# Performance work log

Hardware: AMD Instinct MI355X
Metric: run time of the kernel (lower is better)

## Reference

```python
import jax, jax.numpy as jnp
import numpy as np

B, S, D, H = 2, 2048, 1024, 16
HD = D // H  # head dim = 64


def setup_inputs() -> dict:
    key = jax.random.key(0)
    ks = jax.random.split(key, 8)
    s = 0.02
    return {
        "Q": jax.random.normal(ks[0], (B, S, D), jnp.float32),
        "K": jax.random.normal(ks[1], (B, S, D), jnp.float32),
        "V": jax.random.normal(ks[2], (B, S, D), jnp.float32),
        "mask": jax.random.randint(ks[3], (1, 1, S, S), 0, 2, jnp.int32),
        "Wq": jax.random.normal(ks[4], (D, D), jnp.float32) * s,
        "bq": jnp.zeros((D,), jnp.float32),
        "Wk": jax.random.normal(ks[5], (D, D), jnp.float32) * s,
        "bk": jnp.zeros((D,), jnp.float32),
        "Wv": jax.random.normal(ks[6], (D, D), jnp.float32) * s,
        "bv": jnp.zeros((D,), jnp.float32),
        "Wo": jax.random.normal(ks[7], (D, D), jnp.float32) * s,
        "bo": jnp.zeros((D,), jnp.float32),
    }


def reference(Q, K, V, mask, Wq, bq, Wk, bk, Wv, bv, Wo, bo):
    b = Q.shape[0]
    # QKV projections, split into heads: [B,S,D] -> [B,H,S,HD]
    q = (Q @ Wq + bq).reshape(b, -1, H, HD).transpose(0, 2, 1, 3)
    k = (K @ Wk + bk).reshape(b, -1, H, HD).transpose(0, 2, 1, 3)
    v = (V @ Wv + bv).reshape(b, -1, H, HD).transpose(0, 2, 1, 3)
    # scaled dot-product attention with full [B,H,S,S] scores (as in source)
    scale = jnp.sqrt(jnp.asarray(HD, q.dtype))
    scores = jnp.einsum("bhqd,bhkd->bhqk", q, k) / scale
    scores = jnp.where(mask == 0, -jnp.inf, scores)
    attn = jax.nn.softmax(scores, axis=-1)
    ctx = jnp.einsum("bhqk,bhkd->bhqd", attn, v)
    # merge heads and output projection
    concat = ctx.transpose(0, 2, 1, 3).reshape(b, -1, H * HD)
    return concat @ Wo + bo
```

## Files before the change

kernel.cpp:

```cpp
#include <hip/hip_runtime.h>


using s8v = __attribute__((ext_vector_type(8))) short;
using f4v = __attribute__((ext_vector_type(4))) float;
using f16v = __attribute__((ext_vector_type(16))) float;
typedef unsigned long long u64;

__device__ __forceinline__ unsigned short f2bf(float f) {
  union { float f; unsigned int u; } v; v.f = f;
  return (unsigned short)((v.u + 0x7fffu + ((v.u >> 16) & 1u)) >> 16);
}

__device__ __forceinline__ unsigned pkbf(float lo, float hi2) {
  return __builtin_amdgcn_perm(__float_as_uint(hi2), __float_as_uint(lo), 0x07060302);
}

__device__ __forceinline__ void gll16(const void* g, void* l) {
  __builtin_amdgcn_global_load_lds(
      (const __attribute__((address_space(1))) unsigned int*)g,
      (__attribute__((address_space(3))) unsigned int*)l, 16, 0, 0);
}

__global__ void prep_kernel(const float* __restrict__ Q, const float* __restrict__ K,
                            const float* __restrict__ V,
                            unsigned short* __restrict__ qb, unsigned short* __restrict__ kb,
                            unsigned short* __restrict__ vb,
                            const float* __restrict__ W0, const float* __restrict__ W1,
                            const float* __restrict__ W2, const float* __restrict__ W3,
                            unsigned short* __restrict__ T0, unsigned short* __restrict__ T1,
                            unsigned short* __restrict__ T2, unsigned short* __restrict__ T3,
                            const int* __restrict__ mask, unsigned* __restrict__ bmw) {
  __shared__ unsigned short t[64][72];
  const int bid = blockIdx.x, tid = threadIdx.x;
  if (bid < 1536) {
    int z = bid >> 9;
    int base = (bid & 511) * 2048;
    const float* in = (z == 0) ? Q : (z == 1) ? K : V;
    unsigned short* out = (z == 0) ? qb : (z == 1) ? kb : vb;
#pragma unroll
    for (int j = 0; j < 8; ++j) {
      int idx = base + j * 256 + tid;
      float4 v = ((const float4*)in)[idx];
      ushort4 o;
      o.x = f2bf(v.x); o.y = f2bf(v.y); o.z = f2bf(v.z); o.w = f2bf(v.w);
      ((ushort4*)out)[idx] = o;
    }
  } else if (bid < 2560) {
    int b = bid - 1536;
    int z = b >> 8, rem = b & 255;
    int k0 = (rem >> 4) * 64, n0 = (rem & 15) * 64;
    const float* W = (z == 0) ? W0 : (z == 1) ? W1 : (z == 2) ? W2 : W3;
    unsigned short* Wt = (z == 0) ? T0 : (z == 1) ? T1 : (z == 2) ? T2 : T3;
    for (int p = 0; p < 4; ++p) {
      int idx = p * 256 + tid;
      int row = idx >> 4, c4 = idx & 15;
      float4 v = *(const float4*)&W[(size_t)(k0 + row) * 1024 + n0 + c4 * 4];
      t[row][c4 * 4 + 0] = f2bf(v.x);
      t[row][c4 * 4 + 1] = f2bf(v.y);
      t[row][c4 * 4 + 2] = f2bf(v.z);
      t[row][c4 * 4 + 3] = f2bf(v.w);
    }
    __syncthreads();
    for (int p = 0; p < 2; ++p) {
      int idx = p * 256 + tid;
      int j = idx >> 3, c8 = idx & 7;
      unsigned short tmp[8];
      for (int i = 0; i < 8; ++i) tmp[i] = t[c8 * 8 + i][j];
      uint4 o;
      o.x = tmp[0] | ((unsigned)tmp[1] << 16);
      o.y = tmp[2] | ((unsigned)tmp[3] << 16);
      o.z = tmp[4] | ((unsigned)tmp[5] << 16);
      o.w = tmp[6] | ((unsigned)tmp[7] << 16);
      *(uint4*)&Wt[(size_t)(n0 + j) * 1024 + k0 + c8 * 8] = o;
    }
  } else {
    int b = bid - 2560;
#pragma unroll
    for (int j = 0; j < 8; ++j) {
      int g = b * 2048 + j * 256 + tid;
      int widx = g & 15, hi = (g >> 4) & 1, l31 = (g >> 5) & 31;
      int it = (g >> 10) & 31, rowblk = g >> 15;
      int ni = widx >> 3, kcl = (widx >> 2) & 1, e = widx & 3;
      int kk = 64 * it + 32 * ni + 16 * kcl + 4 * hi + (e >> 1) * 8 + (e & 1) * 2;
      int qrow = rowblk * 32 + l31;
      const int* mrow = mask + (size_t)qrow * 2048 + kk;
      unsigned wd = (mrow[0] ? 0xFFFFu : 0u) | (mrow[1] ? 0xFFFF0000u : 0u);
      bmw[g] = wd;
    }
  }
}

__global__ __launch_bounds__(256) void proj3_kernel(
    const unsigned short* __restrict__ A0, const unsigned short* __restrict__ A1,
    const unsigned short* __restrict__ A2,
    const unsigned short* __restrict__ W0, const unsigned short* __restrict__ W1,
    const unsigned short* __restrict__ W2,
    const float* __restrict__ b0, const float* __restrict__ b1, const float* __restrict__ b2,
    unsigned short* __restrict__ oq, unsigned short* __restrict__ ok,
    unsigned short* __restrict__ ovt) {
  const int orig = blockIdx.z * 256 + blockIdx.y * 32 + blockIdx.x;
  const int swz = (orig & 7) * 96 + (orig >> 3);
  const int z = swz >> 8;
  const int bx = swz & 31, by = (swz >> 5) & 7;

  const unsigned short* A  = (z == 0) ? A0 : (z == 1) ? A1 : A2;
  const unsigned short* Wt = (z == 0) ? W0 : (z == 1) ? W1 : W2;
  const float* bias        = (z == 0) ? b0 : (z == 1) ? b1 : b2;

  __shared__ __align__(16) union SH {
    unsigned short KB[3][8192];
    unsigned short Ls[128][136];
  } sh;

  const int tid = threadIdx.x;
  const int lane = tid & 63, w = tid >> 6, ln = lane & 15, quad = lane >> 4;
  const int wm = (w & 1) * 64, wn = (w >> 1) * 64;
  const int m0 = bx * 128, n0 = by * 128;

  const int slr = lane >> 2;
  const int schunk = (lane & 3) ^ ((lane >> 3) & 3);
  const int cfrag = (quad ^ ((ln >> 1) & 3)) * 8;

  auto STAGE = [&](int buf, int kt) {
    gll16(&A[(size_t)(m0 + w * 32 + slr) * 1024 + kt + schunk * 8],       &sh.KB[buf][(w * 32) * 32]);
    gll16(&A[(size_t)(m0 + w * 32 + 16 + slr) * 1024 + kt + schunk * 8],  &sh.KB[buf][(w * 32 + 16) * 32]);
    gll16(&Wt[(size_t)(n0 + w * 32 + slr) * 1024 + kt + schunk * 8],      &sh.KB[buf][4096 + (w * 32) * 32]);
    gll16(&Wt[(size_t)(n0 + w * 32 + 16 + slr) * 1024 + kt + schunk * 8], &sh.KB[buf][4096 + (w * 32 + 16) * 32]);
  };

  f4v zero = {0.f, 0.f, 0.f, 0.f};
  f4v acc[4][4];
  for (int mi = 0; mi < 4; ++mi)
    for (int ni = 0; ni < 4; ++ni) acc[mi][ni] = zero;

  STAGE(0, 0);
  STAGE(1, 32);
  asm volatile("s_waitcnt vmcnt(4)" ::: "memory");
  __builtin_amdgcn_s_barrier();
  __builtin_amdgcn_sched_barrier(0);

  int cur = 0;
  for (int step = 0; step < 32; ++step) {
    if (step < 30) {
      const int nb = (cur == 0) ? 2 : cur - 1;
      STAGE(nb, step * 32 + 64);
    }
    const unsigned short* Asb = &sh.KB[cur][0];
    const unsigned short* Bsb = &sh.KB[cur][4096];
    s8v a[4], b[4];
    for (int mi = 0; mi < 4; ++mi) a[mi] = *(const s8v*)&Asb[(wm + mi * 16 + ln) * 32 + cfrag];
    for (int ni = 0; ni < 4; ++ni) b[ni] = *(const s8v*)&Bsb[(wn + ni * 16 + ln) * 32 + cfrag];
    if (z < 2) {
      for (int mi = 0; mi < 4; ++mi)
        for (int ni = 0; ni < 4; ++ni)
          acc[mi][ni] = __builtin_amdgcn_mfma_f32_16x16x32_bf16(a[mi], b[ni], acc[mi][ni], 0, 0, 0);
    } else {
      for (int mi = 0; mi < 4; ++mi)
        for (int ni = 0; ni < 4; ++ni)
          acc[mi][ni] = __builtin_amdgcn_mfma_f32_16x16x32_bf16(b[ni], a[mi], acc[mi][ni], 0, 0, 0);
    }
    if (step < 30)       asm volatile("s_waitcnt vmcnt(4)" ::: "memory");
    else if (step == 30) asm volatile("s_waitcnt vmcnt(0)" ::: "memory");
    if (step < 31) {
      __builtin_amdgcn_s_barrier();
      __builtin_amdgcn_sched_barrier(0);
    }
    cur = (cur == 2) ? 0 : cur + 1;
  }
  __syncthreads();

  if (z < 2) {
    const float qscale = (z == 0) ? 0.18033688f : 1.0f;
    for (int mi = 0; mi < 4; ++mi) {
      int row = wm + mi * 16 + quad * 4;
      for (int ni = 0; ni < 4; ++ni) {
        int col = wn + ni * 16 + ln;
        float bvv = bias[n0 + col];
        for (int r = 0; r < 4; ++r)
          sh.Ls[row + r][col] = f2bf((acc[mi][ni][r] + bvv) * qscale);
      }
    }
  } else {
    for (int ni = 0; ni < 4; ++ni) {
      for (int r = 0; r < 4; ++r) {
        int colw = wn + ni * 16 + quad * 4 + r;
        float bvv = bias[n0 + colw];
        for (int mi = 0; mi < 4; ++mi) {
          int rowg = wm + mi * 16 + ln;
          sh.Ls[colw][rowg] = f2bf(acc[mi][ni][r] + bvv);
        }
      }
    }
  }
  __syncthreads();

  if (z < 2) {
    unsigned short* outp = (z == 0) ? oq : ok;
    for (int p = 0; p < 8; ++p) {
      int row = p * 16 + (tid >> 4);
      int cg  = tid & 15;
      uint4 vv = *(const uint4*)&sh.Ls[row][cg * 8];
      int rb = m0 + row, b_ = rb >> 11, s = rb & 2047;
      int colg = n0 + cg * 8, h = colg >> 6, hd = colg & 63;
      *(uint4*)&outp[(((size_t)(b_ * 16 + h)) * 2048 + s) * 64 + hd] = vv;
    }
  } else {
    for (int p = 0; p < 8; ++p) {
      int rr = p * 16 + (tid >> 4);
      int cg = tid & 15;
      uint4 vv = *(const uint4*)&sh.Ls[rr][cg * 8];
      int colw = n0 + rr, h = colw >> 6, hd = colw & 63;
      int sg = m0 + cg * 8, b_ = sg >> 11, ss = sg & 2047;
      *(uint4*)&ovt[(((size_t)(b_ * 16 + h)) * 64 + hd) * 2048 + ss] = vv;
    }
  }
}

#define FLASH_ITER(i, SIN0, SIN1, SOUT0, SOUT1)                                 \
  {                                                                             \
    const int cur = (i) & 1;                                                    \
    uint4 nA, nB, nC, nD;                                                       \
    if ((i) < 31) {                                                             \
      const uint4* m4 = (const uint4*)(mwp + ((i) + 1) * 1024);                 \
      nA = m4[0]; nB = m4[1]; nC = m4[2]; nD = m4[3];                           \
    }                                                                           \
          \
    __builtin_amdgcn_s_setprio(1);                                              \
    if ((i) < 31) {                                                             \
      s8v ak0 = *(const s8v*)&k_s[cur ^ 1][l31][hi * 8];                        \
      s8v ak1 = *(const s8v*)&k_s[cur ^ 1][32 + l31][hi * 8];                   \
      SOUT0 = __builtin_amdgcn_mfma_f32_32x32x16_bf16(ak0, qf[0], zf, 0, 0, 0); \
      SOUT1 = __builtin_amdgcn_mfma_f32_32x32x16_bf16(ak1, qf[0], zf, 0, 0, 0); \
      _Pragma("unroll")                                                         \
      for (int c = 1; c < 4; ++c) {                                             \
        ak0 = *(const s8v*)&k_s[cur ^ 1][l31][c * 16 + hi * 8];                 \
        ak1 = *(const s8v*)&k_s[cur ^ 1][32 + l31][c * 16 + hi * 8];            \
        SOUT0 = __builtin_amdgcn_mfma_f32_32x32x16_bf16(ak0, qf[c], SOUT0, 0, 0, 0); \
        SOUT1 = __builtin_amdgcn_mfma_f32_32x32x16_bf16(ak1, qf[c], SOUT1, 0, 0, 0); \
      }                                                                         \
    }                                                                           \
    __builtin_amdgcn_s_setprio(0);                                              \
         \
    s8v pf[4];                                                                  \
    _Pragma("unroll")                                                           \
    for (int ni = 0; ni < 2; ++ni) {                                            \
      const f16v sv = ni ? SIN1 : SIN0;                                         \
      _Pragma("unroll")                                                         \
      for (int kcl = 0; kcl < 2; ++kcl) {                                       \
        const int rb = 8 * kcl;                                                 \
        const uint4 mw = ni ? (kcl ? mwD : mwC) : (kcl ? mwB : mwA);            \
        unsigned x0 = pkbf(__builtin_amdgcn_exp2f(sv[rb + 0]),                  \
                           __builtin_amdgcn_exp2f(sv[rb + 1])) & mw.x;          \
        unsigned x1 = pkbf(__builtin_amdgcn_exp2f(sv[rb + 2]),                  \
                           __builtin_amdgcn_exp2f(sv[rb + 3])) & mw.y;          \
        unsigned y0 = pkbf(__builtin_amdgcn_exp2f(sv[rb + 4]),                  \
                           __builtin_amdgcn_exp2f(sv[rb + 5])) & mw.z;          \
        unsigned y1 = pkbf(__builtin_amdgcn_exp2f(sv[rb + 6]),                  \
                           __builtin_amdgcn_exp2f(sv[rb + 7])) & mw.w;          \
        asm("v_permlane32_swap_b32 %0, %1" : "+v"(x0), "+v"(y0));               \
        asm("v_permlane32_swap_b32 %0, %1" : "+v"(x1), "+v"(y1));               \
        union { uint4 u; s8v v; } cv;                                           \
        cv.u = make_uint4(x0, x1, y0, y1);                                      \
        pf[ni * 2 + kcl] = cv.v;                                                \
      }                                                                         \
    }                                                                           \
                                              \
    __builtin_amdgcn_s_setprio(1);                                              \
    _Pragma("unroll")                                                           \
    for (int kc = 0; kc < 4; ++kc)                                              \
      lac = __builtin_amdgcn_mfma_f32_32x32x16_bf16(pf[kc], ones, lac, 0, 0, 0);\
    _Pragma("unroll")                                                           \
    for (int kc = 0; kc < 4; ++kc) {                                            \
      s8v bv0 = *(const s8v*)&v_s[cur][l31][kc * 16 + hi * 8];                  \
      s8v bv1 = *(const s8v*)&v_s[cur][32 + l31][kc * 16 + hi * 8];             \
      o0 = __builtin_amdgcn_mfma_f32_32x32x16_bf16(pf[kc], bv0, o0, 0, 0, 0);   \
      o1 = __builtin_amdgcn_mfma_f32_32x32x16_bf16(pf[kc], bv1, o1, 0, 0, 0);   \
    }                                                                           \
    __builtin_amdgcn_s_setprio(0);                                              \
           \
                                \
    __builtin_amdgcn_sched_barrier(0);                                          \
    __builtin_amdgcn_s_barrier();                                               \
    __builtin_amdgcn_sched_barrier(0);                                          \
    if ((i) < 30) WRITET(cur);                         \
    if ((i) < 29) LOADT((i) + 3);         \
     \
    asm volatile("s_waitcnt lgkmcnt(0)" ::: "memory");                          \
    __builtin_amdgcn_sched_barrier(0);                                          \
    __builtin_amdgcn_s_barrier();                                               \
    __builtin_amdgcn_sched_barrier(0);                                          \
    mwA = nA; mwB = nB; mwC = nC; mwD = nD;                                     \
  }

__global__ __launch_bounds__(256, 2) void flash_kernel(
    const unsigned short* __restrict__ q, const unsigned short* __restrict__ k,
    const unsigned short* __restrict__ vt, const unsigned* __restrict__ bmw,
    unsigned short* __restrict__ ctx) {
  __shared__ __align__(16) unsigned short k_s[2][64][72];
  __shared__ __align__(16) unsigned short v_s[2][64][72];

  const int tid = threadIdx.x;
  const int lane = tid & 63, w = tid >> 6;
  const int l31 = lane & 31, hi = lane >> 5;
  const int orig = blockIdx.y * 16 + blockIdx.x;
  const int swzid = (orig & 7) * 64 + (orig >> 3);
  const int bx = swzid & 15, bh = swzid >> 4;
  const int q0 = bx * 128;
  const unsigned short* qg  = q  + ((size_t)bh * 2048 + q0) * 64;
  const unsigned short* kgb = k  + (size_t)bh * 2048 * 64;
  const unsigned short* vgb = vt + (size_t)bh * 64 * 2048;
  const unsigned* mwp = bmw + (size_t)(bx * 4 + w) * 32768 + l31 * 32 + hi * 16;

  const int qrow = w * 32 + l31;
  s8v qf[4];
#pragma unroll
  for (int c = 0; c < 4; ++c)
    qf[c] = *(const s8v*)&qg[(size_t)qrow * 64 + c * 16 + hi * 8];

  s8v ones;
#pragma unroll
  for (int i = 0; i < 8; ++i) ones[i] = (short)0x3F80;
  f16v zf;
#pragma unroll
  for (int i = 0; i < 16; ++i) zf[i] = 0.f;

  const int srow = tid >> 3, sc8 = tid & 7;

  uint4 kr0, kr1, vr0, vr1;
  auto LOADT = [&](int it) {
    const int kk = it * 64;
    kr0 = *(const uint4*)&kgb[(size_t)(kk + srow) * 64 + sc8 * 8];
    kr1 = *(const uint4*)&kgb[(size_t)(kk + srow + 32) * 64 + sc8 * 8];
    vr0 = *(const uint4*)&vgb[(size_t)srow * 2048 + kk + sc8 * 8];
    vr1 = *(const uint4*)&vgb[(size_t)(srow + 32) * 2048 + kk + sc8 * 8];
  };
  auto WRITET = [&](int b) {
    *(uint4*)&k_s[b][srow][sc8 * 8] = kr0;
    *(uint4*)&k_s[b][srow + 32][sc8 * 8] = kr1;
    *(uint4*)&v_s[b][srow][sc8 * 8] = vr0;
    *(uint4*)&v_s[b][srow + 32][sc8 * 8] = vr1;
  };

  LOADT(0); WRITET(0);
  LOADT(1); WRITET(1);
  LOADT(2);
  __syncthreads();

  uint4 mwA, mwB, mwC, mwD;
  {
    const uint4* m4 = (const uint4*)mwp;
    mwA = m4[0]; mwB = m4[1]; mwC = m4[2]; mwD = m4[3];
  }

  f16v sA0, sA1, sB0, sB1;
  {
    s8v ak0 = *(const s8v*)&k_s[0][l31][hi * 8];
    s8v ak1 = *(const s8v*)&k_s[0][32 + l31][hi * 8];
    sA0 = __builtin_amdgcn_mfma_f32_32x32x16_bf16(ak0, qf[0], zf, 0, 0, 0);
    sA1 = __builtin_amdgcn_mfma_f32_32x32x16_bf16(ak1, qf[0], zf, 0, 0, 0);
#pragma unroll
    for (int c = 1; c < 4; ++c) {
      ak0 = *(const s8v*)&k_s[0][l31][c * 16 + hi * 8];
      ak1 = *(const s8v*)&k_s[0][32 + l31][c * 16 + hi * 8];
      sA0 = __builtin_amdgcn_mfma_f32_32x32x16_bf16(ak0, qf[c], sA0, 0, 0, 0);
      sA1 = __builtin_amdgcn_mfma_f32_32x32x16_bf16(ak1, qf[c], sA1, 0, 0, 0);
    }
  }

  f16v o0, o1, lac;
#pragma unroll
  for (int i = 0; i < 16; ++i) { o0[i] = 0.f; o1[i] = 0.f; lac[i] = 0.f; }

  for (int ii = 0; ii < 16; ++ii) {
    const int i0 = ii * 2;
    FLASH_ITER(i0,     sA0, sA1, sB0, sB1);
    FLASH_ITER(i0 + 1, sB0, sB1, sA0, sA1);
  }

  const int b_ = bh >> 4, h = bh & 15;
#pragma unroll
  for (int r = 0; r < 16; ++r) {
    const int ql = (r & 3) + 8 * (r >> 2) + 4 * hi;
    const float inv = 1.f / lac[r];
    const int srw = q0 + w * 32 + ql;
    const size_t base = ((size_t)b_ * 2048 + srw) * 1024 + h * 64;
    ctx[base + l31] = f2bf(o0[r] * inv);
    ctx[base + 32 + l31] = f2bf(o1[r] * inv);
  }
}

__global__ __launch_bounds__(256) void gemm_out_kernel(
    const unsigned short* __restrict__ A, const unsigned short* __restrict__ Wt,
    const float* __restrict__ bias, float* __restrict__ out) {
  __shared__ __align__(16) unsigned short As[3][2048];
  __shared__ __align__(16) unsigned short Bs[3][4096];

  const int tid = threadIdx.x;
  const int lane = tid & 63, w = tid >> 6, ln = lane & 15, quad = lane >> 4;
  const int wm = (w & 1) * 32, wn = (w >> 1) * 64;
  const int orig = blockIdx.y * 64 + blockIdx.x;
  const int swzid = (orig & 7) * 64 + (orig >> 3);
  const int m0 = (swzid & 63) * 64, n0 = (swzid >> 6) * 128;

  const int slr = lane >> 2;
  const int schunk = (lane & 3) ^ ((lane >> 3) & 3);
  const int cfrag = (quad ^ ((ln >> 1) & 3)) * 8;

  auto STAGE = [&](int buf, int kt) {
    gll16(&A[(size_t)(m0 + w * 16 + slr) * 1024 + kt + schunk * 8],       &As[buf][(w * 16) * 32]);
    gll16(&Wt[(size_t)(n0 + w * 32 + slr) * 1024 + kt + schunk * 8],      &Bs[buf][(w * 32) * 32]);
    gll16(&Wt[(size_t)(n0 + w * 32 + 16 + slr) * 1024 + kt + schunk * 8], &Bs[buf][(w * 32 + 16) * 32]);
  };

  f4v zero = {0.f, 0.f, 0.f, 0.f};
  f4v acc[2][4];
  for (int mi = 0; mi < 2; ++mi)
    for (int ni = 0; ni < 4; ++ni) acc[mi][ni] = zero;

  STAGE(0, 0);
  STAGE(1, 32);
  asm volatile("s_waitcnt vmcnt(3)" ::: "memory");
  __builtin_amdgcn_s_barrier();
  __builtin_amdgcn_sched_barrier(0);

  int cur = 0;
  for (int step = 0; step < 32; ++step) {
    if (step < 30) {
      const int nb = (cur == 0) ? 2 : cur - 1;
      STAGE(nb, step * 32 + 64);
    }
    s8v a[2], b[4];
    for (int mi = 0; mi < 2; ++mi) a[mi] = *(const s8v*)&As[cur][(wm + mi * 16 + ln) * 32 + cfrag];
    for (int ni = 0; ni < 4; ++ni) b[ni] = *(const s8v*)&Bs[cur][(wn + ni * 16 + ln) * 32 + cfrag];
    for (int mi = 0; mi < 2; ++mi)
      for (int ni = 0; ni < 4; ++ni)
        acc[mi][ni] = __builtin_amdgcn_mfma_f32_16x16x32_bf16(a[mi], b[ni], acc[mi][ni], 0, 0, 0);
    if (step < 30)       asm volatile("s_waitcnt vmcnt(3)" ::: "memory");
    else if (step == 30) asm volatile("s_waitcnt vmcnt(0)" ::: "memory");
    if (step < 31) {
      __builtin_amdgcn_s_barrier();
      __builtin_amdgcn_sched_barrier(0);
    }
    cur = (cur == 2) ? 0 : cur + 1;
  }

  for (int mi = 0; mi < 2; ++mi) {
    int rb = m0 + wm + mi * 16 + quad * 4;
    for (int ni = 0; ni < 4; ++ni) {
      int col = n0 + wn + ni * 16 + ln;
      float bvv = bias[col];
      for (int r = 0; r < 4; ++r)
        out[(size_t)(rb + r) * 1024 + col] = acc[mi][ni][r] + bvv;
    }
  }
}

extern "C" void kernel_launch(void* const* d_in, const int* in_sizes, int n_in,
                              void* d_out, int out_size, void* d_ws, size_t ws_size,
                              hipStream_t stream) {
  const float* Q  = (const float*)d_in[0];
  const float* K  = (const float*)d_in[1];
  const float* V  = (const float*)d_in[2];
  const int* mask = (const int*)d_in[3];
  const float* Wq = (const float*)d_in[4];
  const float* bq = (const float*)d_in[5];
  const float* Wk = (const float*)d_in[6];
  const float* bk = (const float*)d_in[7];
  const float* Wv = (const float*)d_in[8];
  const float* bv = (const float*)d_in[9];
  const float* Wo = (const float*)d_in[10];
  const float* bo = (const float*)d_in[11];
  float* out = (float*)d_out;

  char* ws = (char*)d_ws;
  const size_t MB = 1u << 20;
  unsigned short* qb  = (unsigned short*)(ws + 0 * MB);
  unsigned short* kb  = (unsigned short*)(ws + 8 * MB);
  unsigned short* vb  = (unsigned short*)(ws + 16 * MB);
  unsigned short* wqt = (unsigned short*)(ws + 24 * MB);
  unsigned short* wkt = (unsigned short*)(ws + 26 * MB);
  unsigned short* wvt = (unsigned short*)(ws + 28 * MB);
  unsigned short* wot = (unsigned short*)(ws + 30 * MB);
  unsigned short* qh  = (unsigned short*)(ws + 32 * MB);
  unsigned short* kh  = (unsigned short*)(ws + 40 * MB);
  unsigned short* vth = (unsigned short*)(ws + 48 * MB);
  unsigned* bmw       = (unsigned*)(ws + 56 * MB);
  unsigned short* ctx = (unsigned short*)(ws + 16 * MB);

  prep_kernel<<<3584, 256, 0, stream>>>(Q, K, V, qb, kb, vb,
                                        Wq, Wk, Wv, Wo, wqt, wkt, wvt, wot,
                                        mask, bmw);
  proj3_kernel<<<dim3(32, 8, 3), 256, 0, stream>>>(qb, kb, vb, wqt, wkt, wvt,
                                                   bq, bk, bv, qh, kh, vth);
  flash_kernel<<<dim3(16, 32), 256, 0, stream>>>(qh, kh, vth, bmw, ctx);
  gemm_out_kernel<<<dim3(64, 8), 256, 0, stream>>>(ctx, wot, bo, out);
}
```

Baseline: 245.8 us.

## Process 128-key tiles per flash iteration with separate K and V staging

```diff
diff --git a/kernel.cpp b/kernel.cpp
--- a/kernel.cpp
+++ b/kernel.cpp
@@ -216,39 +216,15 @@
   }
 }
 
-#define FLASH_ITER(i, SIN0, SIN1, SOUT0, SOUT1)                                 \
+#define PACK64(S0V, S1V, MA, MB, MC, MD, PF)                                    \
   {                                                                             \
-    const int cur = (i) & 1;                                                    \
-    uint4 nA, nB, nC, nD;                                                       \
-    if ((i) < 31) {                                                             \
-      const uint4* m4 = (const uint4*)(mwp + ((i) + 1) * 1024);                 \
-      nA = m4[0]; nB = m4[1]; nC = m4[2]; nD = m4[3];                           \
-    }                                                                           \
-          \
-    __builtin_amdgcn_s_setprio(1);                                              \
-    if ((i) < 31) {                                                             \
-      s8v ak0 = *(const s8v*)&k_s[cur ^ 1][l31][hi * 8];                        \
-      s8v ak1 = *(const s8v*)&k_s[cur ^ 1][32 + l31][hi * 8];                   \
-      SOUT0 = __builtin_amdgcn_mfma_f32_32x32x16_bf16(ak0, qf[0], zf, 0, 0, 0); \
-      SOUT1 = __builtin_amdgcn_mfma_f32_32x32x16_bf16(ak1, qf[0], zf, 0, 0, 0); \
-      _Pragma("unroll")                                                         \
-      for (int c = 1; c < 4; ++c) {                                             \
-        ak0 = *(const s8v*)&k_s[cur ^ 1][l31][c * 16 + hi * 8];                 \
-        ak1 = *(const s8v*)&k_s[cur ^ 1][32 + l31][c * 16 + hi * 8];            \
-        SOUT0 = __builtin_amdgcn_mfma_f32_32x32x16_bf16(ak0, qf[c], SOUT0, 0, 0, 0); \
-        SOUT1 = __builtin_amdgcn_mfma_f32_32x32x16_bf16(ak1, qf[c], SOUT1, 0, 0, 0); \
-      }                                                                         \
-    }                                                                           \
-    __builtin_amdgcn_s_setprio(0);                                              \
-         \
-    s8v pf[4];                                                                  \
     _Pragma("unroll")                                                           \
     for (int ni = 0; ni < 2; ++ni) {                                            \
-      const f16v sv = ni ? SIN1 : SIN0;                                         \
+      const f16v sv = ni ? S1V : S0V;                                           \
       _Pragma("unroll")                                                         \
       for (int kcl = 0; kcl < 2; ++kcl) {                                       \
         const int rb = 8 * kcl;                                                 \
-        const uint4 mw = ni ? (kcl ? mwD : mwC) : (kcl ? mwB : mwA);            \
+        const uint4 mw = ni ? (kcl ? MD : MC) : (kcl ? MB : MA);                \
         unsigned x0 = pkbf(__builtin_amdgcn_exp2f(sv[rb + 0]),                  \
                            __builtin_amdgcn_exp2f(sv[rb + 1])) & mw.x;          \
         unsigned x1 = pkbf(__builtin_amdgcn_exp2f(sv[rb + 2]),                  \
@@ -261,43 +237,17 @@
         asm("v_permlane32_swap_b32 %0, %1" : "+v"(x1), "+v"(y1));               \
         union { uint4 u; s8v v; } cv;                                           \
         cv.u = make_uint4(x0, x1, y0, y1);                                      \
-        pf[ni * 2 + kcl] = cv.v;                                                \
+        PF[ni * 2 + kcl] = cv.v;                                                \
       }                                                                         \
     }                                                                           \
-                                              \
-    __builtin_amdgcn_s_setprio(1);                                              \
-    _Pragma("unroll")                                                           \
-    for (int kc = 0; kc < 4; ++kc)                                              \
-      lac = __builtin_amdgcn_mfma_f32_32x32x16_bf16(pf[kc], ones, lac, 0, 0, 0);\
-    _Pragma("unroll")                                                           \
-    for (int kc = 0; kc < 4; ++kc) {                                            \
-      s8v bv0 = *(const s8v*)&v_s[cur][l31][kc * 16 + hi * 8];                  \
-      s8v bv1 = *(const s8v*)&v_s[cur][32 + l31][kc * 16 + hi * 8];             \
-      o0 = __builtin_amdgcn_mfma_f32_32x32x16_bf16(pf[kc], bv0, o0, 0, 0, 0);   \
-      o1 = __builtin_amdgcn_mfma_f32_32x32x16_bf16(pf[kc], bv1, o1, 0, 0, 0);   \
-    }                                                                           \
-    __builtin_amdgcn_s_setprio(0);                                              \
-           \
-                                \
-    __builtin_amdgcn_sched_barrier(0);                                          \
-    __builtin_amdgcn_s_barrier();                                               \
-    __builtin_amdgcn_sched_barrier(0);                                          \
-    if ((i) < 30) WRITET(cur);                         \
-    if ((i) < 29) LOADT((i) + 3);         \
-     \
-    asm volatile("s_waitcnt lgkmcnt(0)" ::: "memory");                          \
-    __builtin_amdgcn_sched_barrier(0);                                          \
-    __builtin_amdgcn_s_barrier();                                               \
-    __builtin_amdgcn_sched_barrier(0);                                          \
-    mwA = nA; mwB = nB; mwC = nC; mwD = nD;                                     \
   }
 
 __global__ __launch_bounds__(256, 2) void flash_kernel(
     const unsigned short* __restrict__ q, const unsigned short* __restrict__ k,
     const unsigned short* __restrict__ vt, const unsigned* __restrict__ bmw,
     unsigned short* __restrict__ ctx) {
-  __shared__ __align__(16) unsigned short k_s[2][64][72];
-  __shared__ __align__(16) unsigned short v_s[2][64][72];
+  __shared__ __align__(16) unsigned short k_s[2][128][72];
+  __shared__ __align__(16) unsigned short v_s[64][136];
 
   const int tid = threadIdx.x;
   const int lane = tid & 63, w = tid >> 6;
@@ -326,55 +276,127 @@
 
   const int srow = tid >> 3, sc8 = tid & 7;
 
-  uint4 kr0, kr1, vr0, vr1;
-  auto LOADT = [&](int it) {
-    const int kk = it * 64;
+  uint4 kr0, kr1, kr2, kr3, vr0, vr1, vr2, vr3;
+  auto LOADK = [&](int it) {
+    const int kk = it * 128;
     kr0 = *(const uint4*)&kgb[(size_t)(kk + srow) * 64 + sc8 * 8];
     kr1 = *(const uint4*)&kgb[(size_t)(kk + srow + 32) * 64 + sc8 * 8];
-    vr0 = *(const uint4*)&vgb[(size_t)srow * 2048 + kk + sc8 * 8];
-    vr1 = *(const uint4*)&vgb[(size_t)(srow + 32) * 2048 + kk + sc8 * 8];
+    kr2 = *(const uint4*)&kgb[(size_t)(kk + srow + 64) * 64 + sc8 * 8];
+    kr3 = *(const uint4*)&kgb[(size_t)(kk + srow + 96) * 64 + sc8 * 8];
   };
-  auto WRITET = [&](int b) {
+  auto WRITEK = [&](int b) {
     *(uint4*)&k_s[b][srow][sc8 * 8] = kr0;
     *(uint4*)&k_s[b][srow + 32][sc8 * 8] = kr1;
-    *(uint4*)&v_s[b][srow][sc8 * 8] = vr0;
-    *(uint4*)&v_s[b][srow + 32][sc8 * 8] = vr1;
+    *(uint4*)&k_s[b][srow + 64][sc8 * 8] = kr2;
+    *(uint4*)&k_s[b][srow + 96][sc8 * 8] = kr3;
   };
-
-  LOADT(0); WRITET(0);
-  LOADT(1); WRITET(1);
-  LOADT(2);
+  auto LOADV = [&](int it) {
+    const int kk = it * 128;
+    vr0 = *(const uint4*)&vgb[(size_t)srow * 2048 + kk + sc8 * 8];
+    vr1 = *(const uint4*)&vgb[(size_t)srow * 2048 + kk + 64 + sc8 * 8];
+    vr2 = *(const uint4*)&vgb[(size_t)(srow + 32) * 2048 + kk + sc8 * 8];
+    vr3 = *(const uint4*)&vgb[(size_t)(srow + 32) * 2048 + kk + 64 + sc8 * 8];
+  };
+  auto WRITEV = [&]() {
+    *(uint4*)&v_s[srow][sc8 * 8] = vr0;
+    *(uint4*)&v_s[srow][64 + sc8 * 8] = vr1;
+    *(uint4*)&v_s[srow + 32][sc8 * 8] = vr2;
+    *(uint4*)&v_s[srow + 32][64 + sc8 * 8] = vr3;
+  };
+
+  LOADK(0); LOADV(0);
+  WRITEK(0); WRITEV();
+  LOADK(1); LOADV(1);
   __syncthreads();
 
-  uint4 mwA, mwB, mwC, mwD;
-  {
-    const uint4* m4 = (const uint4*)mwp;
-    mwA = m4[0]; mwB = m4[1]; mwC = m4[2]; mwD = m4[3];
-  }
-
-  f16v sA0, sA1, sB0, sB1;
-  {
-    s8v ak0 = *(const s8v*)&k_s[0][l31][hi * 8];
-    s8v ak1 = *(const s8v*)&k_s[0][32 + l31][hi * 8];
-    sA0 = __builtin_amdgcn_mfma_f32_32x32x16_bf16(ak0, qf[0], zf, 0, 0, 0);
-    sA1 = __builtin_amdgcn_mfma_f32_32x32x16_bf16(ak1, qf[0], zf, 0, 0, 0);
-#pragma unroll
-    for (int c = 1; c < 4; ++c) {
-      ak0 = *(const s8v*)&k_s[0][l31][c * 16 + hi * 8];
-      ak1 = *(const s8v*)&k_s[0][32 + l31][c * 16 + hi * 8];
-      sA0 = __builtin_amdgcn_mfma_f32_32x32x16_bf16(ak0, qf[c], sA0, 0, 0, 0);
-      sA1 = __builtin_amdgcn_mfma_f32_32x32x16_bf16(ak1, qf[c], sA1, 0, 0, 0);
-    }
-  }
-
   f16v o0, o1, lac;
 #pragma unroll
   for (int i = 0; i < 16; ++i) { o0[i] = 0.f; o1[i] = 0.f; lac[i] = 0.f; }
 
-  for (int ii = 0; ii < 16; ++ii) {
-    const int i0 = ii * 2;
-    FLASH_ITER(i0,     sA0, sA1, sB0, sB1);
-    FLASH_ITER(i0 + 1, sB0, sB1, sA0, sA1);
+  int cur = 0;
+  for (int i = 0; i < 16; ++i) {
+    const uint4* m4a = (const uint4*)(mwp + (2 * i) * 1024);
+    const uint4 m0A = m4a[0], m0B = m4a[1], m0C = m4a[2], m0D = m4a[3];
+    const uint4* m4b = (const uint4*)(mwp + (2 * i + 1) * 1024);
+    const uint4 m1A = m4b[0], m1B = m4b[1], m1C = m4b[2], m1D = m4b[3];
+
+    __builtin_amdgcn_s_setprio(1);
+    f16v s00, s01;
+    {
+      s8v ak0 = *(const s8v*)&k_s[cur][l31][hi * 8];
+      s8v ak1 = *(const s8v*)&k_s[cur][32 + l31][hi * 8];
+      s00 = __builtin_amdgcn_mfma_f32_32x32x16_bf16(ak0, qf[0], zf, 0, 0, 0);
+      s01 = __builtin_amdgcn_mfma_f32_32x32x16_bf16(ak1, qf[0], zf, 0, 0, 0);
+#pragma unroll
+      for (int c = 1; c < 4; ++c) {
+        ak0 = *(const s8v*)&k_s[cur][l31][c * 16 + hi * 8];
+        ak1 = *(const s8v*)&k_s[cur][32 + l31][c * 16 + hi * 8];
+        s00 = __builtin_amdgcn_mfma_f32_32x32x16_bf16(ak0, qf[c], s00, 0, 0, 0);
+        s01 = __builtin_amdgcn_mfma_f32_32x32x16_bf16(ak1, qf[c], s01, 0, 0, 0);
+      }
+    }
+    f16v s10, s11;
+    {
+      s8v ak0 = *(const s8v*)&k_s[cur][64 + l31][hi * 8];
+      s8v ak1 = *(const s8v*)&k_s[cur][96 + l31][hi * 8];
+      s10 = __builtin_amdgcn_mfma_f32_32x32x16_bf16(ak0, qf[0], zf, 0, 0, 0);
+      s11 = __builtin_amdgcn_mfma_f32_32x32x16_bf16(ak1, qf[0], zf, 0, 0, 0);
+#pragma unroll
+      for (int c = 1; c < 4; ++c) {
+        ak0 = *(const s8v*)&k_s[cur][64 + l31][c * 16 + hi * 8];
+        ak1 = *(const s8v*)&k_s[cur][96 + l31][c * 16 + hi * 8];
+        s10 = __builtin_amdgcn_mfma_f32_32x32x16_bf16(ak0, qf[c], s10, 0, 0, 0);
+        s11 = __builtin_amdgcn_mfma_f32_32x32x16_bf16(ak1, qf[c], s11, 0, 0, 0);
+      }
+    }
+    __builtin_amdgcn_s_setprio(0);
+
+    if (i < 15) WRITEK(cur ^ 1);
+    if (i < 14) LOADK(i + 2);
+
+    s8v pf[4];
+    PACK64(s00, s01, m0A, m0B, m0C, m0D, pf);
+    __builtin_amdgcn_s_setprio(1);
+#pragma unroll
+    for (int kc = 0; kc < 4; ++kc)
+      lac = __builtin_amdgcn_mfma_f32_32x32x16_bf16(pf[kc], ones, lac, 0, 0, 0);
+#pragma unroll
+    for (int kc = 0; kc < 4; ++kc) {
+      s8v bv0 = *(const s8v*)&v_s[l31][kc * 16 + hi * 8];
+      s8v bv1 = *(const s8v*)&v_s[32 + l31][kc * 16 + hi * 8];
+      o0 = __builtin_amdgcn_mfma_f32_32x32x16_bf16(pf[kc], bv0, o0, 0, 0, 0);
+      o1 = __builtin_amdgcn_mfma_f32_32x32x16_bf16(pf[kc], bv1, o1, 0, 0, 0);
+    }
+    __builtin_amdgcn_s_setprio(0);
+
+    s8v pg[4];
+    PACK64(s10, s11, m1A, m1B, m1C, m1D, pg);
+    __builtin_amdgcn_s_setprio(1);
+#pragma unroll
+    for (int kc = 0; kc < 4; ++kc)
+      lac = __builtin_amdgcn_mfma_f32_32x32x16_bf16(pg[kc], ones, lac, 0, 0, 0);
+#pragma unroll
+    for (int kc = 0; kc < 4; ++kc) {
+      s8v bv0 = *(const s8v*)&v_s[l31][64 + kc * 16 + hi * 8];
+      s8v bv1 = *(const s8v*)&v_s[32 + l31][64 + kc * 16 + hi * 8];
+      o0 = __builtin_amdgcn_mfma_f32_32x32x16_bf16(pg[kc], bv0, o0, 0, 0, 0);
+      o1 = __builtin_amdgcn_mfma_f32_32x32x16_bf16(pg[kc], bv1, o1, 0, 0, 0);
+    }
+    __builtin_amdgcn_s_setprio(0);
+
+    if (i < 15) {
+      asm volatile("s_waitcnt lgkmcnt(0)" ::: "memory");
+      __builtin_amdgcn_sched_barrier(0);
+      __builtin_amdgcn_s_barrier();
+      __builtin_amdgcn_sched_barrier(0);
+      WRITEV();
+      if (i < 14) LOADV(i + 2);
+      asm volatile("s_waitcnt lgkmcnt(0)" ::: "memory");
+      __builtin_amdgcn_sched_barrier(0);
+      __builtin_amdgcn_s_barrier();
+      __builtin_amdgcn_sched_barrier(0);
+    }
+    cur ^= 1;
   }
 
   const int b_ = bh >> 4, h = bh & 15;
```

After: 251.5 us. +2.3%, slower.
